# Kernel optimization log

Hardware: AMD Instinct MI355X
Metric: run time of the kernel (lower is better)

## Reference

```python
import jax, jax.numpy as jnp
import numpy as np

N_NODES = 131072
N_EDGES = 1048576
N_GRAPHS = 1024
EMB = 96
HID = 64
OUT = 3
NEG_SLOPE = 0.2  # PyG GATConv default leaky_relu slope


def setup_inputs() -> dict:
    key = jax.random.key(0)
    ks = jax.random.split(key, 8)
    x = jax.random.normal(ks[0], (N_NODES, EMB), dtype=jnp.float32)
    edge_index = jax.random.randint(ks[1], (2, N_EDGES), 0, N_NODES, dtype=jnp.int64)
    batch = jnp.sort(jax.random.randint(ks[2], (N_NODES,), 0, N_GRAPHS, dtype=jnp.int64))
    s = 1.0 / np.sqrt(EMB)
    W = jax.random.uniform(ks[3], (EMB, HID), jnp.float32, -s, s)       # GATConv lin (no bias)
    att_src = jax.random.uniform(ks[4], (HID,), jnp.float32, -s, s)     # a_src
    att_dst = jax.random.uniform(ks[5], (HID,), jnp.float32, -s, s)     # a_dst
    bias_gat = jnp.zeros((HID,), jnp.float32)
    sf = 1.0 / np.sqrt(HID)
    fc_w = jax.random.uniform(ks[6], (OUT, HID), jnp.float32, -sf, sf)
    fc_b = jax.random.uniform(ks[7], (OUT,), jnp.float32, -sf, sf)
    return {"x": x, "edge_index": edge_index, "batch": batch, "W": W,
            "att_src": att_src, "att_dst": att_dst, "bias_gat": bias_gat,
            "fc_w": fc_w, "fc_b": fc_b}


def _segment_softmax(logits, seg, num_segments):
    # numerically stable softmax over edges grouped by target node
    m = jax.ops.segment_max(logits, seg, num_segments=num_segments)
    e = jnp.exp(logits - m[seg])
    z = jax.ops.segment_sum(e, seg, num_segments=num_segments)
    return e / (z[seg] + 1e-16)


def reference(x, edge_index, batch, W, att_src, att_dst, bias_gat, fc_w, fc_b):
    N = x.shape[0]
    # PyG GATConv (heads=1): add self loops
    loop = jnp.arange(N, dtype=edge_index.dtype)
    src = jnp.concatenate([edge_index[0], loop])
    dst = jnp.concatenate([edge_index[1], loop])

    h = x @ W                                    # [N, HID]
    a_s = h @ att_src                            # [N]
    a_d = h @ att_dst                            # [N]
    logits = jax.nn.leaky_relu(a_s[src] + a_d[dst], NEG_SLOPE)  # [E]
    alpha = _segment_softmax(logits, dst, N)     # softmax over in-edges per target
    out = jax.ops.segment_sum(alpha[:, None] * h[src], dst, num_segments=N)
    out = out + bias_gat                         # [N, HID]

    # global_mean_pool over graphs
    sums = jax.ops.segment_sum(out, batch, num_segments=N_GRAPHS)
    cnt = jax.ops.segment_sum(jnp.ones((N,), out.dtype), batch, num_segments=N_GRAPHS)
    pooled = sums / jnp.maximum(cnt, 1.0)[:, None]  # [G, HID]

    logits_out = pooled @ fc_w.T + fc_b          # [G, OUT]
    return jax.nn.log_softmax(logits_out, axis=1)
```

## Files before the change

kernel.cpp:

```cpp
#include <hip/hip_runtime.h>
#include <hip/hip_fp16.h>

#define N_NODES 131072
#define N_EDGES 1048576
#define N_GRAPHS 1024
#define EMB 96
#define HID 64
#define CAP 32
#define NBKT 128
#define NCHUNK 1024
#define BCAP2 32

typedef _Float16 half8 __attribute__((ext_vector_type(8)));
typedef float float4v __attribute__((ext_vector_type(4)));

__global__ __launch_bounds__(256) void k_bucket(const int* __restrict__ src,
    const int* __restrict__ dst, int2* __restrict__ ebuf, int* __restrict__ ccnt,
    const float* __restrict__ W, _Float16* __restrict__ Wt)
{
    int tid = threadIdx.x;
    int blk = blockIdx.x;
    __shared__ int bcnt[NBKT];
    if (tid < NBKT) bcnt[tid] = 0;
    if (blk < 24) {
        int t = blk * 256 + tid;
        Wt[(t & 63) * EMB + (t >> 6)] = (_Float16)W[t];
    }
    __syncthreads();
    int e0 = blk * 1024;
    #pragma unroll
    for (int i = 0; i < 4; ++i) {
        int e = e0 + i * 256 + tid;
        int sv = src[e], dv = dst[e];
        int b = dv >> 10;
        int r = atomicAdd(&bcnt[b], 1);
        if (r < BCAP2)
            ebuf[((size_t)b * NCHUNK + blk) * BCAP2 + r] = make_int2(sv, dv);
    }
    __syncthreads();
    if (tid < NBKT) {
        int v = bcnt[tid];
        ccnt[tid * NCHUNK + blk] = v < BCAP2 ? v : BCAP2;
    }
}

__global__ __launch_bounds__(512, 4) void k_lin_place(
    const float* __restrict__ x, const _Float16* __restrict__ Wt,
    const float* __restrict__ att_src, const float* __restrict__ att_dst,
    __half* __restrict__ h, float* __restrict__ a_s, float* __restrict__ a_d,
    const int2* __restrict__ ebuf, const int* __restrict__ ccnt,
    int* __restrict__ cnt, int* __restrict__ slots,
    float* __restrict__ pool, float* __restrict__ gcnt)
{
    int tid = threadIdx.x;
    __shared__ int cl[1024];
    __shared__ int cm[1024];

    if (blockIdx.x < NBKT) {
        int b = blockIdx.x;
        cl[tid] = 0; cl[tid + 512] = 0;
        cm[tid] = ccnt[b * NCHUNK + tid];
        cm[tid + 512] = ccnt[b * NCHUNK + 512 + tid];
        pool[b * 512 + tid] = 0.f;
        if (b == 0) { gcnt[tid] = 0.f; gcnt[tid + 512] = 0.f; }
        __syncthreads();
        int lane = tid & 63;
        int w = tid >> 6;
        int half = lane >> 5;
        int s32 = lane & 31;
        const int2* eb = ebuf + (size_t)b * NCHUNK * BCAP2;
        for (int it0 = 0; it0 < 64; it0 += 8) {
            int2 e[8];
            #pragma unroll
            for (int k = 0; k < 8; ++k) {
                int c = w * 128 + (it0 + k) * 2 + half;
                e[k] = eb[c * BCAP2 + s32];
            }
            #pragma unroll
            for (int k = 0; k < 8; ++k) {
                int c = w * 128 + (it0 + k) * 2 + half;
                if (s32 < cm[c]) {
                    int slot = atomicAdd(&cl[e[k].y & 1023], 1);
                    if (slot < CAP) slots[(size_t)e[k].y * CAP + slot] = e[k].x;
                }
            }
        }
        __syncthreads();
        cnt[b * 1024 + tid] = cl[tid];
        cnt[b * 1024 + 512 + tid] = cl[tid + 512];
    } else {
        int sub = blockIdx.x - NBKT;
        int lane = tid & 63;
        int w = tid >> 6;
        int m16 = lane & 15;
        int quad = lane >> 4;
        int rowbase = sub * 128 + w * 16;

        half8 bf[4][3];
        #pragma unroll
        for (int nt = 0; nt < 4; ++nt)
            #pragma unroll
            for (int kb = 0; kb < 3; ++kb)
                bf[nt][kb] = *(const half8*)(Wt + (nt * 16 + m16) * EMB
                                             + kb * 32 + quad * 8);

        float4v acc[4];
        #pragma unroll
        for (int nt = 0; nt < 4; ++nt)
            acc[nt] = (float4v){0.f, 0.f, 0.f, 0.f};

        const float* xrow = x + (size_t)(rowbase + m16) * EMB + quad * 8;
        #pragma unroll
        for (int kb = 0; kb < 3; ++kb) {
            float4 xa = *(const float4*)(xrow + kb * 32);
            float4 xb = *(const float4*)(xrow + kb * 32 + 4);
            half8 af;
            af[0] = (_Float16)xa.x; af[1] = (_Float16)xa.y;
            af[2] = (_Float16)xa.z; af[3] = (_Float16)xa.w;
            af[4] = (_Float16)xb.x; af[5] = (_Float16)xb.y;
            af[6] = (_Float16)xb.z; af[7] = (_Float16)xb.w;
            #pragma unroll
            for (int nt = 0; nt < 4; ++nt)
                acc[nt] = __builtin_amdgcn_mfma_f32_16x16x32_f16(
                    af, bf[nt][kb], acc[nt], 0, 0, 0);
        }

        float asv[4], adv[4];
        #pragma unroll
        for (int nt = 0; nt < 4; ++nt) {
            asv[nt] = att_src[nt * 16 + m16];
            adv[nt] = att_dst[nt * 16 + m16];
        }

        #pragma unroll
        for (int r = 0; r < 4; ++r) {
            int row = rowbase + quad * 4 + r;
            float ps = 0.f, pd = 0.f;
            #pragma unroll
            for (int nt = 0; nt < 4; ++nt) {
                float v = acc[nt][r];
                h[(size_t)row * HID + nt * 16 + m16] = __float2half(v);
                ps += v * asv[nt];
                pd += v * adv[nt];
            }
            #pragma unroll
            for (int off = 8; off >= 1; off >>= 1) {
                ps += __shfl_xor(ps, off, 64);
                pd += __shfl_xor(pd, off, 64);
            }
            if (m16 == 0) { a_s[row] = ps; a_d[row] = pd; }
        }
    }
}

__global__ __launch_bounds__(256) void k_accum(const __half2* __restrict__ h2,
    const float* __restrict__ a_s, const float* __restrict__ a_d,
    const int* __restrict__ cnt, const int* __restrict__ slots,
    const float* __restrict__ bias, __half2* __restrict__ out)
{
    int tid = threadIdx.x;
    int lane = tid & 63;
    int sub = lane & 31;
    int gbase = lane & 32;
    int node = blockIdx.x * 8 + ((tid >> 6) << 1) + (gbase >> 5);

    int deg = cnt[node]; if (deg > CAP) deg = CAP;
    float adi = a_d[node];
    float asi = a_s[node];

    int s_j = node;
    if (sub < deg) s_j = slots[(size_t)node * CAP + sub];
    float t = a_s[s_j] + adi;
    t = t > 0.f ? t : 0.2f * t;
    float w_j = (sub < deg) ? __expf(t) : 0.f;

    float t0 = asi + adi;
    t0 = t0 > 0.f ? t0 : 0.2f * t0;
    float w0 = __expf(t0);

    float z = w_j;
    #pragma unroll
    for (int off = 16; off >= 1; off >>= 1) z += __shfl_xor(z, off, 64);
    z += w0;

    __half2 hv = h2[(size_t)node * 32 + sub];
    float2 acc;
    acc.x = w0 * __half2float(hv.x);
    acc.y = w0 * __half2float(hv.y);

    int iters = (deg + 3) >> 2;
    for (int it = 0; it < iters; ++it) {
        int j = it * 4;
        int i0 = __shfl(s_j, gbase + j,     64);
        int i1 = __shfl(s_j, gbase + j + 1, 64);
        int i2 = __shfl(s_j, gbase + j + 2, 64);
        int i3 = __shfl(s_j, gbase + j + 3, 64);
        float w0_ = __shfl(w_j, gbase + j,     64);
        float w1_ = __shfl(w_j, gbase + j + 1, 64);
        float w2_ = __shfl(w_j, gbase + j + 2, 64);
        float w3_ = __shfl(w_j, gbase + j + 3, 64);
        __half2 g0 = h2[(size_t)i0 * 32 + sub];
        __half2 g1 = h2[(size_t)i1 * 32 + sub];
        __half2 g2 = h2[(size_t)i2 * 32 + sub];
        __half2 g3 = h2[(size_t)i3 * 32 + sub];
        acc.x += w0_ * __half2float(g0.x) + w1_ * __half2float(g1.x)
               + w2_ * __half2float(g2.x) + w3_ * __half2float(g3.x);
        acc.y += w0_ * __half2float(g0.y) + w1_ * __half2float(g1.y)
               + w2_ * __half2float(g2.y) + w3_ * __half2float(g3.y);
    }

    float inv = 1.f / (z + 1e-16f);
    float2 b2 = ((const float2*)bias)[sub];
    out[(size_t)node * 32 + sub] =
        __floats2half2_rn(acc.x * inv + b2.x, acc.y * inv + b2.y);
}

__global__ __launch_bounds__(256) void k_pool(const __half* __restrict__ out,
    const int* __restrict__ batch, float* __restrict__ pool,
    float* __restrict__ gcnt)
{
    int lane = threadIdx.x & 63;
    int wv = blockIdx.x * 4 + (threadIdx.x >> 6);
    int base = wv * 64;
    int bv = batch[base + lane];
    int g_cur = __shfl(bv, 0);
    float acc = 0.f;
    int run = 0;
    for (int c = 0; c < 8; ++c) {
        int n0 = base + c * 8;
        float v[8];
        #pragma unroll
        for (int k = 0; k < 8; ++k)
            v[k] = __half2float(out[(size_t)(n0 + k) * HID + lane]);
        int b0 = __shfl(bv, c * 8);
        int b7 = __shfl(bv, c * 8 + 7);
        if (b0 == b7) {
            if (b0 != g_cur) {
                atomicAdd(&pool[g_cur * HID + lane], acc);
                if (lane == 0) atomicAdd(&gcnt[g_cur], (float)run);
                acc = 0.f; run = 0; g_cur = b0;
            }
            acc += ((v[0] + v[1]) + (v[2] + v[3]))
                 + ((v[4] + v[5]) + (v[6] + v[7]));
            run += 8;
        } else {
            #pragma unroll
            for (int k = 0; k < 8; ++k) {
                int g = __shfl(bv, c * 8 + k);
                if (g != g_cur) {
                    atomicAdd(&pool[g_cur * HID + lane], acc);
                    if (lane == 0) atomicAdd(&gcnt[g_cur], (float)run);
                    acc = 0.f; run = 0; g_cur = g;
                }
                acc += v[k]; ++run;
            }
        }
    }
    atomicAdd(&pool[g_cur * HID + lane], acc);
    if (lane == 0) atomicAdd(&gcnt[g_cur], (float)run);
}

__global__ __launch_bounds__(256) void k_head(const float* __restrict__ pool,
    const float* __restrict__ gcnt, const float* __restrict__ fc_w,
    const float* __restrict__ fc_b, float* __restrict__ out)
{
    int tid = threadIdx.x;
    int lane = tid & 63;
    int g = blockIdx.x * 4 + (tid >> 6);
    float p = pool[g * HID + lane] / fmaxf(gcnt[g], 1.0f);
    float l0 = p * fc_w[0 * HID + lane];
    float l1 = p * fc_w[1 * HID + lane];
    float l2 = p * fc_w[2 * HID + lane];
    #pragma unroll
    for (int off = 32; off >= 1; off >>= 1) {
        l0 += __shfl_xor(l0, off, 64);
        l1 += __shfl_xor(l1, off, 64);
        l2 += __shfl_xor(l2, off, 64);
    }
    l0 += fc_b[0]; l1 += fc_b[1]; l2 += fc_b[2];
    float m = fmaxf(l0, fmaxf(l1, l2));
    float lse = m + logf(__expf(l0 - m) + __expf(l1 - m) + __expf(l2 - m));
    if (lane == 0) {
        out[g * 3 + 0] = l0 - lse;
        out[g * 3 + 1] = l1 - lse;
        out[g * 3 + 2] = l2 - lse;
    }
}

extern "C" void kernel_launch(void* const* d_in, const int* in_sizes, int n_in,
                              void* d_out, int out_size, void* d_ws, size_t ws_size,
                              hipStream_t stream)
{
    const float* x        = (const float*)d_in[0];
    const int*   ei       = (const int*)d_in[1];
    const int*   batch    = (const int*)d_in[2];
    const float* W        = (const float*)d_in[3];
    const float* att_src  = (const float*)d_in[4];
    const float* att_dst  = (const float*)d_in[5];
    const float* bias_gat = (const float*)d_in[6];
    const float* fc_w     = (const float*)d_in[7];
    const float* fc_b     = (const float*)d_in[8];
    float* out = (float*)d_out;

    char* ws = (char*)d_ws;
    size_t off = 0;
    auto alloc = [&](size_t bytes) {
        void* p = ws + off;
        off += (bytes + 255) & ~(size_t)255;
        return p;
    };
    __half* h    = (__half*)alloc((size_t)N_NODES * HID * 2);
    int*   slots = (int*)  alloc((size_t)N_NODES * CAP * 4);
    int*   cnt   = (int*)  alloc((size_t)N_NODES * 4);
    int*   ccnt  = (int*)  alloc((size_t)NCHUNK * NBKT * 4);
    float* a_s   = (float*)alloc((size_t)N_NODES * 4);
    float* a_d   = (float*)alloc((size_t)N_NODES * 4);
    float* pool  = (float*)alloc((size_t)N_GRAPHS * HID * 4);
    float* gcnt  = (float*)alloc((size_t)N_GRAPHS * 4);
    _Float16* Wt = (_Float16*)alloc((size_t)HID * EMB * 2);
    int2*  ebuf  = (int2*)alloc((size_t)NBKT * NCHUNK * BCAP2 * 8);
    __half* nout = (__half*)ebuf;

    const int* e_src = ei;
    const int* e_dst = ei + N_EDGES;

    k_bucket<<<NCHUNK, 256, 0, stream>>>(e_src, e_dst, ebuf, ccnt, W, Wt);
    k_lin_place<<<NBKT + 1024, 512, 0, stream>>>(x, Wt, att_src, att_dst,
                                                 h, a_s, a_d, ebuf, ccnt,
                                                 cnt, slots, pool, gcnt);
    k_accum <<<N_NODES / 8, 256, 0, stream>>>((const __half2*)h, a_s, a_d, cnt,
                                              slots, bias_gat, (__half2*)nout);
    k_pool  <<<N_NODES / 256, 256, 0, stream>>>(nout, batch, pool, gcnt);
    k_head  <<<N_GRAPHS / 4, 256, 0, stream>>>(pool, gcnt, fc_w, fc_b, out);
}
```

Baseline: 188.3 us.

## Pack bucketed edges into one int and prefetch neighbor rows in accumulation

Edge records in the bucket buffer are packed into a single int (src shifted left by 10, plus the low 10 bits of dst) instead of an int2. This halves the scratch traffic written by k_bucket and read by k_lin_place. k_accum now issues 16 neighbor-row gathers up front, before the softmax weights are computed, to hide gather latency. Degrees above 16 are handled in chunks of 8, and the kernel gets an occupancy hint. The cost is redundant loads of the node's own row for low-degree nodes and higher register pressure.

Result: faster. 181.7 us (-3.5%).

```diff
diff --git a/kernel.cpp b/kernel.cpp
--- a/kernel.cpp
+++ b/kernel.cpp
@@ -15,7 +15,7 @@
 typedef float float4v __attribute__((ext_vector_type(4)));
 
 __global__ __launch_bounds__(256) void k_bucket(const int* __restrict__ src,
-    const int* __restrict__ dst, int2* __restrict__ ebuf, int* __restrict__ ccnt,
+    const int* __restrict__ dst, int* __restrict__ ebuf, int* __restrict__ ccnt,
     const float* __restrict__ W, _Float16* __restrict__ Wt)
 {
     int tid = threadIdx.x;
@@ -35,7 +35,7 @@
         int b = dv >> 10;
         int r = atomicAdd(&bcnt[b], 1);
         if (r < BCAP2)
-            ebuf[((size_t)b * NCHUNK + blk) * BCAP2 + r] = make_int2(sv, dv);
+            ebuf[((size_t)b * NCHUNK + blk) * BCAP2 + r] = (sv << 10) | (dv & 1023);
     }
     __syncthreads();
     if (tid < NBKT) {
@@ -48,7 +48,7 @@
     const float* __restrict__ x, const _Float16* __restrict__ Wt,
     const float* __restrict__ att_src, const float* __restrict__ att_dst,
     __half* __restrict__ h, float* __restrict__ a_s, float* __restrict__ a_d,
-    const int2* __restrict__ ebuf, const int* __restrict__ ccnt,
+    const int* __restrict__ ebuf, const int* __restrict__ ccnt,
     int* __restrict__ cnt, int* __restrict__ slots,
     float* __restrict__ pool, float* __restrict__ gcnt)
 {
@@ -68,9 +68,10 @@
         int w = tid >> 6;
         int half = lane >> 5;
         int s32 = lane & 31;
-        const int2* eb = ebuf + (size_t)b * NCHUNK * BCAP2;
+        const int* eb = ebuf + (size_t)b * NCHUNK * BCAP2;
+        int bbase = b << 10;
         for (int it0 = 0; it0 < 64; it0 += 8) {
-            int2 e[8];
+            int e[8];
             #pragma unroll
             for (int k = 0; k < 8; ++k) {
                 int c = w * 128 + (it0 + k) * 2 + half;
@@ -80,8 +81,10 @@
             for (int k = 0; k < 8; ++k) {
                 int c = w * 128 + (it0 + k) * 2 + half;
                 if (s32 < cm[c]) {
-                    int slot = atomicAdd(&cl[e[k].y & 1023], 1);
-                    if (slot < CAP) slots[(size_t)e[k].y * CAP + slot] = e[k].x;
+                    int local = e[k] & 1023;
+                    int slot = atomicAdd(&cl[local], 1);
+                    if (slot < CAP)
+                        slots[(size_t)(bbase | local) * CAP + slot] = e[k] >> 10;
                 }
             }
         }
@@ -153,7 +156,7 @@
     }
 }
 
-__global__ __launch_bounds__(256) void k_accum(const __half2* __restrict__ h2,
+__global__ __launch_bounds__(256, 6) void k_accum(const __half2* __restrict__ h2,
     const float* __restrict__ a_s, const float* __restrict__ a_d,
     const int* __restrict__ cnt, const int* __restrict__ slots,
     const float* __restrict__ bias, __half2* __restrict__ out)
@@ -165,12 +168,21 @@
     int node = blockIdx.x * 8 + ((tid >> 6) << 1) + (gbase >> 5);
 
     int deg = cnt[node]; if (deg > CAP) deg = CAP;
+    int s_j = node;
+    if (sub < deg) s_j = slots[(size_t)node * CAP + sub];
+
+    __half2 hv = h2[(size_t)node * 32 + sub];
+    __half2 hg[16];
+    #pragma unroll
+    for (int k = 0; k < 16; ++k) {
+        int i = __shfl(s_j, gbase + k, 64);
+        hg[k] = h2[(size_t)i * 32 + sub];
+    }
+    float asg = a_s[s_j];
     float adi = a_d[node];
     float asi = a_s[node];
 
-    int s_j = node;
-    if (sub < deg) s_j = slots[(size_t)node * CAP + sub];
-    float t = a_s[s_j] + adi;
+    float t = asg + adi;
     t = t > 0.f ? t : 0.2f * t;
     float w_j = (sub < deg) ? __expf(t) : 0.f;
 
@@ -183,30 +195,29 @@
     for (int off = 16; off >= 1; off >>= 1) z += __shfl_xor(z, off, 64);
     z += w0;
 
-    __half2 hv = h2[(size_t)node * 32 + sub];
     float2 acc;
     acc.x = w0 * __half2float(hv.x);
     acc.y = w0 * __half2float(hv.y);
-
-    int iters = (deg + 3) >> 2;
-    for (int it = 0; it < iters; ++it) {
-        int j = it * 4;
-        int i0 = __shfl(s_j, gbase + j,     64);
-        int i1 = __shfl(s_j, gbase + j + 1, 64);
-        int i2 = __shfl(s_j, gbase + j + 2, 64);
-        int i3 = __shfl(s_j, gbase + j + 3, 64);
-        float w0_ = __shfl(w_j, gbase + j,     64);
-        float w1_ = __shfl(w_j, gbase + j + 1, 64);
-        float w2_ = __shfl(w_j, gbase + j + 2, 64);
-        float w3_ = __shfl(w_j, gbase + j + 3, 64);
-        __half2 g0 = h2[(size_t)i0 * 32 + sub];
-        __half2 g1 = h2[(size_t)i1 * 32 + sub];
-        __half2 g2 = h2[(size_t)i2 * 32 + sub];
-        __half2 g3 = h2[(size_t)i3 * 32 + sub];
-        acc.x += w0_ * __half2float(g0.x) + w1_ * __half2float(g1.x)
-               + w2_ * __half2float(g2.x) + w3_ * __half2float(g3.x);
-        acc.y += w0_ * __half2float(g0.y) + w1_ * __half2float(g1.y)
-               + w2_ * __half2float(g2.y) + w3_ * __half2float(g3.y);
+    #pragma unroll
+    for (int k = 0; k < 16; ++k) {
+        float wk = __shfl(w_j, gbase + k, 64);
+        acc.x += wk * __half2float(hg[k].x);
+        acc.y += wk * __half2float(hg[k].y);
+    }
+
+    for (int j0 = 16; j0 < deg; j0 += 8) {
+        __half2 g2[8];
+        #pragma unroll
+        for (int k = 0; k < 8; ++k) {
+            int i = __shfl(s_j, gbase + j0 + k, 64);
+            g2[k] = h2[(size_t)i * 32 + sub];
+        }
+        #pragma unroll
+        for (int k = 0; k < 8; ++k) {
+            float wk = __shfl(w_j, gbase + j0 + k, 64);
+            acc.x += wk * __half2float(g2[k].x);
+            acc.y += wk * __half2float(g2[k].y);
+        }
     }
 
     float inv = 1.f / (z + 1e-16f);
@@ -318,7 +329,7 @@
     float* pool  = (float*)alloc((size_t)N_GRAPHS * HID * 4);
     float* gcnt  = (float*)alloc((size_t)N_GRAPHS * 4);
     _Float16* Wt = (_Float16*)alloc((size_t)HID * EMB * 2);
-    int2*  ebuf  = (int2*)alloc((size_t)NBKT * NCHUNK * BCAP2 * 8);
+    int*   ebuf  = (int*)alloc((size_t)NBKT * NCHUNK * BCAP2 * 4);
     __half* nout = (__half*)ebuf;
 
     const int* e_src = ei;
```
